# Kernel tuning notes

Measured on AMD Instinct MI355X. Metric: run time of the kernel, lower is better.

Reference implementation:

```python
import jax, jax.numpy as jnp
import numpy as np

B, F, C_IN, C_OUT, W_DIM, K2, PAD = 4, 98304, 256, 3, 512, 4, 4096
N = B * F  # total real faces across batch


def setup_inputs() -> dict:
    key = jax.random.key(0)
    ks = jax.random.split(key, 5)
    x = jax.random.normal(ks[0], (N, C_IN), jnp.float32)
    face_neighborhood = jax.random.randint(ks[1], (N, K2), 0, N + PAD)
    # pads placed at the end of the padded slot array (exactly PAD true entries)
    face_is_pad = jnp.concatenate([jnp.zeros((N,), bool), jnp.ones((PAD,), bool)])
    w = jax.random.normal(ks[2], (B, W_DIM), jnp.float32)
    affine_weight = jax.random.normal(ks[3], (C_IN, W_DIM), jnp.float32)
    affine_bias = jnp.ones((C_IN,), jnp.float32)  # bias_init=1
    weight = jax.random.normal(ks[4], (C_OUT, C_IN, 1, K2), jnp.float32)
    bias = jnp.zeros((C_OUT,), jnp.float32)
    return dict(x=x, face_neighborhood=face_neighborhood, face_is_pad=face_is_pad,
                pad_size=PAD, w=w, affine_weight=affine_weight,
                affine_bias=affine_bias, weight=weight, bias=bias)


def reference(x, face_neighborhood, face_is_pad, pad_size, w,
              affine_weight, affine_bias, weight, bias):
    weight_gain = 1.0 / np.sqrt(C_IN * K2)
    # FullyConnectedLayer (stylegan2-ada): out = w @ (A.T / sqrt(in)) + bias(=1)
    styles = (w @ (affine_weight.T / np.float32(np.sqrt(W_DIM))) + affine_bias) * weight_gain  # [B, C_in]
    # create_faceconv_input: scatter real features into padded slots (pads = 0)
    real_rank = jnp.cumsum(~face_is_pad) - 1                      # [N+pad] rank among real slots
    padded = jnp.where(face_is_pad[:, None], jnp.float32(0),
                       x[jnp.clip(real_rank, 0, N - 1)])           # [N+pad, C_in]
    gathered = padded[face_neighborhood]                           # [N, K2, C_in]
    g = gathered.reshape(B, F, K2, C_IN)
    # modulated_face_conv, demodulate=False:
    # out[b,f,o] = sum_{c,k} g[b,f,k,c] * weight[o,c,0,k] * styles[b,c]
    out = jnp.einsum('bfkc,ock,bc->bfo', g, weight[:, :, 0, :], styles)
    out = out.reshape(N, C_OUT) + bias[None, :]
    return jnp.clip(out, -256.0, 256.0)
```

## Files before the change

kernel.cpp:

```cpp
#include <hip/hip_runtime.h>
#include <hip/hip_bf16.h>


#define N_FACES    393216
#define C_IN       256
#define C_OUT      3
#define W_DIM      512
#define K2         4
#define BATCH      4
#define F_PER_B    98304
#define NJ         48
#define ZSLOTS     64
#define PAD        4096
#define REAL_TILES 24576
#define TOT_TILES  24832
#define GEMM_BLOCKS 1536

typedef __attribute__((ext_vector_type(8))) short bf16x8;
typedef __attribute__((ext_vector_type(4))) float f32x4;

static __device__ __forceinline__ float bfbits2f(unsigned int hi16) {
    union { unsigned int u; float f; } v; v.u = hi16;
    return v.f;
}

__global__ __launch_bounds__(256) void wmod_bf16_kernel(
    const float* __restrict__ w,
    const float* __restrict__ aw,
    const float* __restrict__ ab,
    const float* __restrict__ weight,
    unsigned short* __restrict__ wmodT)
{
    int t = blockIdx.x * blockDim.x + threadIdx.x;
    if (t >= BATCH * C_IN) return;
    int b = t >> 8;
    int c = t & 255;

    const float* wr = w  + b * W_DIM;
    const float* ar = aw + c * W_DIM;
    float acc = 0.f;
    #pragma unroll 4
    for (int d = 0; d < W_DIM; d += 4) {
        float4 wv = *reinterpret_cast<const float4*>(wr + d);
        float4 av = *reinterpret_cast<const float4*>(ar + d);
        acc += wv.x * av.x + wv.y * av.y + wv.z * av.z + wv.w * av.w;
    }
    const float rsqrt_wdim = 0.04419417382415922f;
    const float gain       = 0.03125f;
    float s = (acc * rsqrt_wdim + ab[c]) * gain;

    #pragma unroll
    for (int o = 0; o < C_OUT; ++o)
        #pragma unroll
        for (int k = 0; k < K2; ++k) {
            int j = b * (K2 * C_OUT) + k * C_OUT + o;
            union { __hip_bfloat16 h; unsigned short u; } cv;
            cv.h = __float2bfloat16(weight[(o * C_IN + c) * K2 + k] * s);
            wmodT[j * C_IN + c] = cv.u;
        }
}

#define LDW 264

__global__ __launch_bounds__(256) void gemm_z_kernel(
    const float*          __restrict__ x,
    const unsigned short* __restrict__ wmodT,
    unsigned short*       __restrict__ z)
{
    __shared__ __align__(16) unsigned short bs[NJ][LDW];

    const unsigned int* g = reinterpret_cast<const unsigned int*>(wmodT);
    for (int i = threadIdx.x; i < NJ * (C_IN / 2); i += 256) {
        int r = i >> 7;
        int c = i & 127;
        reinterpret_cast<unsigned int*>(&bs[r][0])[c] = g[r * 128 + c];
    }
    __syncthreads();

    const int wave = threadIdx.x >> 6;
    const int lane = threadIdx.x & 63;
    const int row  = lane & 15;
    const int kq   = lane >> 4;
    const int colj = lane & 15;

    int slot[3];
    #pragma unroll
    for (int a = 0; a < 3; ++a) {
        int j   = a * 16 + colj;
        int b   = j / 12;
        int rem = j - b * 12;
        slot[a] = b * 16 + rem + rem / 3;
    }

    for (int gt = blockIdx.x * 4 + wave; gt < TOT_TILES; gt += GEMM_BLOCKS * 4) {
        if (gt < REAL_TILES) {
            const float* xrow = x + (size_t)(gt * 16 + row) * C_IN + kq * 8;

            f32x4 acc0 = {0.f, 0.f, 0.f, 0.f};
            f32x4 acc1 = {0.f, 0.f, 0.f, 0.f};
            f32x4 acc2 = {0.f, 0.f, 0.f, 0.f};

            #pragma unroll
            for (int ks = 0; ks < 8; ++ks) {
                const float4* p = reinterpret_cast<const float4*>(xrow + ks * 32);
                float4 a0 = p[0];
                float4 a1 = p[1];
                union { bf16x8 v; __hip_bfloat16 h[8]; } af;
                af.h[0] = __float2bfloat16(a0.x); af.h[1] = __float2bfloat16(a0.y);
                af.h[2] = __float2bfloat16(a0.z); af.h[3] = __float2bfloat16(a0.w);
                af.h[4] = __float2bfloat16(a1.x); af.h[5] = __float2bfloat16(a1.y);
                af.h[6] = __float2bfloat16(a1.z); af.h[7] = __float2bfloat16(a1.w);

                const int cofs = ks * 32 + kq * 8;
                bf16x8 b0 = *reinterpret_cast<const bf16x8*>(&bs[ 0 + row][cofs]);
                bf16x8 b1 = *reinterpret_cast<const bf16x8*>(&bs[16 + row][cofs]);
                bf16x8 b2 = *reinterpret_cast<const bf16x8*>(&bs[32 + row][cofs]);

                acc0 = __builtin_amdgcn_mfma_f32_16x16x32_bf16(af.v, b0, acc0, 0, 0, 0);
                acc1 = __builtin_amdgcn_mfma_f32_16x16x32_bf16(af.v, b1, acc1, 0, 0, 0);
                acc2 = __builtin_amdgcn_mfma_f32_16x16x32_bf16(af.v, b2, acc2, 0, 0, 0);
            }

            #pragma unroll
            for (int r = 0; r < 4; ++r) {
                size_t zr = (size_t)(gt * 16 + kq * 4 + r) * ZSLOTS;
                union { __hip_bfloat16 h; unsigned short u; } c0, c1, c2;
                c0.h = __float2bfloat16(acc0[r]);
                c1.h = __float2bfloat16(acc1[r]);
                c2.h = __float2bfloat16(acc2[r]);
                z[zr + slot[0]] = c0.u;
                z[zr + slot[1]] = c1.u;
                z[zr + slot[2]] = c2.u;
            }
        } else {
            unsigned short* zp = z + (size_t)(gt * 16 + (lane >> 2)) * ZSLOTS
                                   + (lane & 3) * 16;
            uint4 zero = {0u, 0u, 0u, 0u};
            *reinterpret_cast<uint4*>(zp)     = zero;
            *reinterpret_cast<uint4*>(zp + 8) = zero;
        }
    }
}

__global__ __launch_bounds__(256) void gather_out_kernel(
    const int*            __restrict__ nb,
    const unsigned short* __restrict__ z,
    const float*          __restrict__ bias,
    float*                __restrict__ out)
{
    int n = blockIdx.x * 256 + threadIdx.x;
    if (n >= N_FACES) return;
    int b = n / F_PER_B;

    const int4 idx4 = *reinterpret_cast<const int4*>(nb + n * K2);
    int ids[K2] = { idx4.x, idx4.y, idx4.z, idx4.w };

    float s0 = 0.f, s1 = 0.f, s2 = 0.f;
    #pragma unroll
    for (int k = 0; k < K2; ++k) {
        uint2 v = *reinterpret_cast<const uint2*>(
            z + (size_t)ids[k] * ZSLOTS + b * 16 + k * 4);
        s0 += bfbits2f(v.x << 16);
        s1 += bfbits2f(v.x & 0xffff0000u);
        s2 += bfbits2f(v.y << 16);
    }
    s0 = fminf(fmaxf(s0 + bias[0], -256.f), 256.f);
    s1 = fminf(fmaxf(s1 + bias[1], -256.f), 256.f);
    s2 = fminf(fmaxf(s2 + bias[2], -256.f), 256.f);
    float* po = out + (size_t)n * C_OUT;
    po[0] = s0; po[1] = s1; po[2] = s2;
}

__global__ __launch_bounds__(256) void wmod_kernel(
    const float* __restrict__ w, const float* __restrict__ aw,
    const float* __restrict__ ab, const float* __restrict__ weight,
    float* __restrict__ wmod)
{
    int t = blockIdx.x * blockDim.x + threadIdx.x;
    if (t >= BATCH * C_IN) return;
    int b = t >> 8, c = t & 255;
    const float* wr = w + b * W_DIM;
    const float* ar = aw + c * W_DIM;
    float acc = 0.f;
    #pragma unroll 4
    for (int d = 0; d < W_DIM; d += 4) {
        float4 wv = *reinterpret_cast<const float4*>(wr + d);
        float4 av = *reinterpret_cast<const float4*>(ar + d);
        acc += wv.x * av.x + wv.y * av.y + wv.z * av.z + wv.w * av.w;
    }
    float s = (acc * 0.04419417382415922f + ab[c]) * 0.03125f;
    #pragma unroll
    for (int o = 0; o < C_OUT; ++o)
        #pragma unroll
        for (int k = 0; k < K2; ++k)
            wmod[(((b * K2 + k) * C_OUT + o) << 8) + c] =
                weight[(o * C_IN + c) * K2 + k] * s;
}

__global__ __launch_bounds__(256) void face_conv_kernel(
    const float* __restrict__ x, const int* __restrict__ nb,
    const float* __restrict__ wmod, const float* __restrict__ bias,
    float* __restrict__ out)
{
    const int n    = (blockIdx.x * blockDim.x + threadIdx.x) >> 6;
    const int lane = threadIdx.x & 63;
    if (n >= N_FACES) return;
    const int b = n / F_PER_B;
    const int4 idx4 = *reinterpret_cast<const int4*>(nb + n * K2);
    int idx[K2] = { idx4.x, idx4.y, idx4.z, idx4.w };
    const int cofs = lane << 2;
    const float* wm = wmod + ((b * K2 * C_OUT) << 8) + cofs;
    float acc0 = 0.f, acc1 = 0.f, acc2 = 0.f;
    #pragma unroll
    for (int k = 0; k < K2; ++k) {
        const int id = idx[k];
        if (id < N_FACES) {
            const float4 xv = *reinterpret_cast<const float4*>(x + (size_t)id * C_IN + cofs);
            const float* wk = wm + ((k * C_OUT) << 8);
            const float4 w0 = *reinterpret_cast<const float4*>(wk);
            const float4 w1 = *reinterpret_cast<const float4*>(wk + 256);
            const float4 w2 = *reinterpret_cast<const float4*>(wk + 512);
            acc0 += xv.x * w0.x + xv.y * w0.y + xv.z * w0.z + xv.w * w0.w;
            acc1 += xv.x * w1.x + xv.y * w1.y + xv.z * w1.z + xv.w * w1.w;
            acc2 += xv.x * w2.x + xv.y * w2.y + xv.z * w2.z + xv.w * w2.w;
        }
    }
    #pragma unroll
    for (int off = 32; off > 0; off >>= 1) {
        acc0 += __shfl_xor(acc0, off, 64);
        acc1 += __shfl_xor(acc1, off, 64);
        acc2 += __shfl_xor(acc2, off, 64);
    }
    if (lane < C_OUT) {
        float v = (lane == 0) ? acc0 : (lane == 1) ? acc1 : acc2;
        v += bias[lane];
        v = fminf(fmaxf(v, -256.f), 256.f);
        out[n * C_OUT + lane] = v;
    }
}

extern "C" void kernel_launch(void* const* d_in, const int* in_sizes, int n_in,
                              void* d_out, int out_size, void* d_ws, size_t ws_size,
                              hipStream_t stream)
{
    const float* x      = (const float*)d_in[0];
    const int*   nb     = (const int*)  d_in[1];
    const float* w      = (const float*)d_in[4];
    const float* aw     = (const float*)d_in[5];
    const float* ab     = (const float*)d_in[6];
    const float* weight = (const float*)d_in[7];
    const float* bias   = (const float*)d_in[8];
    float*       out    = (float*)d_out;

    const size_t zoff   = 32768;
    const size_t zbytes = (size_t)TOT_TILES * 16 * ZSLOTS * sizeof(unsigned short);

    if (ws_size >= zoff + zbytes) {
        unsigned short* wmodT = (unsigned short*)d_ws;
        unsigned short* z     = (unsigned short*)((char*)d_ws + zoff);

        wmod_bf16_kernel<<<(BATCH * C_IN + 255) / 256, 256, 0, stream>>>(
            w, aw, ab, weight, wmodT);

        gemm_z_kernel<<<GEMM_BLOCKS, 256, 0, stream>>>(x, wmodT, z);

        gather_out_kernel<<<N_FACES / 256, 256, 0, stream>>>(nb, z, bias, out);
    } else {
        float* wmod = (float*)d_ws;
        wmod_kernel<<<(BATCH * C_IN + 255) / 256, 256, 0, stream>>>(
            w, aw, ab, weight, wmod);
        face_conv_kernel<<<N_FACES / 4, 256, 0, stream>>>(x, nb, wmod, bias, out);
    }
}
```

Before: 145.4 us.

## Stage x tiles through swizzled LDS and keep modulated weights in registers

The GEMM kernel no longer copies the modulated weight matrix into shared memory. Each wave now holds its B fragments in registers, 24 bf16x8 vectors per lane. x tiles are loaded row by row with fully coalesced float4 reads, converted to bf16 and written into a per-wave XOR-swizzled LDS buffer, then read back as MFMA A fragments. The grid shrinks from 1536 to 512 blocks, so each wave processes more tiles and the register-resident weights are reused more. The trade-off is higher register pressure and an extra LDS round trip per tile, with no explicit synchronization between waves.

New measurement: 178.2 us. +22.5%, slower.

```diff
diff --git a/kernel.cpp b/kernel.cpp
--- a/kernel.cpp
+++ b/kernel.cpp
@@ -11,10 +11,10 @@
 #define F_PER_B    98304
 #define NJ         48
 #define ZSLOTS     64
-#define PAD        4096
 #define REAL_TILES 24576
 #define TOT_TILES  24832
-#define GEMM_BLOCKS 1536
+#define GEMM_BLOCKS 512
+#define GRID_WAVES  (GEMM_BLOCKS * 4)
 
 typedef __attribute__((ext_vector_type(8))) short bf16x8;
 typedef __attribute__((ext_vector_type(4))) float f32x4;
@@ -22,6 +22,11 @@
 static __device__ __forceinline__ float bfbits2f(unsigned int hi16) {
     union { unsigned int u; float f; } v; v.u = hi16;
     return v.f;
+}
+static __device__ __forceinline__ unsigned short f2bfu(float f) {
+    union { __hip_bfloat16 h; unsigned short u; } cv;
+    cv.h = __float2bfloat16(f);
+    return cv.u;
 }
 
 __global__ __launch_bounds__(256) void wmod_bf16_kernel(
@@ -54,28 +59,16 @@
         #pragma unroll
         for (int k = 0; k < K2; ++k) {
             int j = b * (K2 * C_OUT) + k * C_OUT + o;
-            union { __hip_bfloat16 h; unsigned short u; } cv;
-            cv.h = __float2bfloat16(weight[(o * C_IN + c) * K2 + k] * s);
-            wmodT[j * C_IN + c] = cv.u;
+            wmodT[j * C_IN + c] = f2bfu(weight[(o * C_IN + c) * K2 + k] * s);
         }
 }
-
-#define LDW 264
 
 __global__ __launch_bounds__(256) void gemm_z_kernel(
     const float*          __restrict__ x,
     const unsigned short* __restrict__ wmodT,
     unsigned short*       __restrict__ z)
 {
-    __shared__ __align__(16) unsigned short bs[NJ][LDW];
-
-    const unsigned int* g = reinterpret_cast<const unsigned int*>(wmodT);
-    for (int i = threadIdx.x; i < NJ * (C_IN / 2); i += 256) {
-        int r = i >> 7;
-        int c = i & 127;
-        reinterpret_cast<unsigned int*>(&bs[r][0])[c] = g[r * 128 + c];
-    }
-    __syncthreads();
+    __shared__ __align__(16) unsigned short xb[4][4096];
 
     const int wave = threadIdx.x >> 6;
     const int lane = threadIdx.x & 63;
@@ -83,6 +76,16 @@
     const int kq   = lane >> 4;
     const int colj = lane & 15;
 
+    char* xw = reinterpret_cast<char*>(&xb[wave][0]);
+
+    bf16x8 bf[3][8];
+    #pragma unroll
+    for (int a = 0; a < 3; ++a)
+        #pragma unroll
+        for (int ks = 0; ks < 8; ++ks)
+            bf[a][ks] = *reinterpret_cast<const bf16x8*>(
+                wmodT + (a * 16 + colj) * C_IN + ks * 32 + kq * 8);
+
     int slot[3];
     #pragma unroll
     for (int a = 0; a < 3; ++a) {
@@ -92,9 +95,20 @@
         slot[a] = b * 16 + rem + rem / 3;
     }
 
-    for (int gt = blockIdx.x * 4 + wave; gt < TOT_TILES; gt += GEMM_BLOCKS * 4) {
+    const int wid = blockIdx.x * 4 + wave;
+    for (int gt = wid; gt < TOT_TILES; gt += GRID_WAVES) {
         if (gt < REAL_TILES) {
-            const float* xrow = x + (size_t)(gt * 16 + row) * C_IN + kq * 8;
+            const float* xt = x + (size_t)gt * 16 * C_IN;
+
+            #pragma unroll
+            for (int j = 0; j < 16; ++j) {
+                float4 v = reinterpret_cast<const float4*>(xt + j * C_IN)[lane];
+                union { unsigned short u[4]; uint2 d; } pk;
+                pk.u[0] = f2bfu(v.x); pk.u[1] = f2bfu(v.y);
+                pk.u[2] = f2bfu(v.z); pk.u[3] = f2bfu(v.w);
+                const int boff = j * 512 + ((lane * 8) ^ ((j & 7) << 4));
+                *reinterpret_cast<uint2*>(xw + boff) = pk.d;
+            }
 
             f32x4 acc0 = {0.f, 0.f, 0.f, 0.f};
             f32x4 acc1 = {0.f, 0.f, 0.f, 0.f};
@@ -102,35 +116,19 @@
 
             #pragma unroll
             for (int ks = 0; ks < 8; ++ks) {
-                const float4* p = reinterpret_cast<const float4*>(xrow + ks * 32);
-                float4 a0 = p[0];
-                float4 a1 = p[1];
-                union { bf16x8 v; __hip_bfloat16 h[8]; } af;
-                af.h[0] = __float2bfloat16(a0.x); af.h[1] = __float2bfloat16(a0.y);
-                af.h[2] = __float2bfloat16(a0.z); af.h[3] = __float2bfloat16(a0.w);
-                af.h[4] = __float2bfloat16(a1.x); af.h[5] = __float2bfloat16(a1.y);
-                af.h[6] = __float2bfloat16(a1.z); af.h[7] = __float2bfloat16(a1.w);
-
-                const int cofs = ks * 32 + kq * 8;
-                bf16x8 b0 = *reinterpret_cast<const bf16x8*>(&bs[ 0 + row][cofs]);
-                bf16x8 b1 = *reinterpret_cast<const bf16x8*>(&bs[16 + row][cofs]);
-                bf16x8 b2 = *reinterpret_cast<const bf16x8*>(&bs[32 + row][cofs]);
-
-                acc0 = __builtin_amdgcn_mfma_f32_16x16x32_bf16(af.v, b0, acc0, 0, 0, 0);
-                acc1 = __builtin_amdgcn_mfma_f32_16x16x32_bf16(af.v, b1, acc1, 0, 0, 0);
-                acc2 = __builtin_amdgcn_mfma_f32_16x16x32_bf16(af.v, b2, acc2, 0, 0, 0);
+                const int aoff = row * 512 + ((ks * 64 + kq * 16) ^ ((row & 7) << 4));
+                bf16x8 av = *reinterpret_cast<const bf16x8*>(xw + aoff);
+                acc0 = __builtin_amdgcn_mfma_f32_16x16x32_bf16(av, bf[0][ks], acc0, 0, 0, 0);
+                acc1 = __builtin_amdgcn_mfma_f32_16x16x32_bf16(av, bf[1][ks], acc1, 0, 0, 0);
+                acc2 = __builtin_amdgcn_mfma_f32_16x16x32_bf16(av, bf[2][ks], acc2, 0, 0, 0);
             }
 
             #pragma unroll
             for (int r = 0; r < 4; ++r) {
                 size_t zr = (size_t)(gt * 16 + kq * 4 + r) * ZSLOTS;
-                union { __hip_bfloat16 h; unsigned short u; } c0, c1, c2;
-                c0.h = __float2bfloat16(acc0[r]);
-                c1.h = __float2bfloat16(acc1[r]);
-                c2.h = __float2bfloat16(acc2[r]);
-                z[zr + slot[0]] = c0.u;
-                z[zr + slot[1]] = c1.u;
-                z[zr + slot[2]] = c2.u;
+                z[zr + slot[0]] = f2bfu(acc0[r]);
+                z[zr + slot[1]] = f2bfu(acc1[r]);
+                z[zr + slot[2]] = f2bfu(acc2[r]);
             }
         } else {
             unsigned short* zp = z + (size_t)(gt * 16 + (lane >> 2)) * ZSLOTS
```
